# Kernel optimization log

Measured on AMD Instinct MI355X. Metric: run time of the kernel, lower is better.

Reference implementation:

```python
import jax, jax.numpy as jnp
import numpy as np

MU = 0.1            # sinkhorn_mu
SINKHORN_ITERS = 200  # fixed-iteration stand-in for tol=1e-9 loop
M_PTS = 4096
N_PTS = 4096


def l2norm(x, eps=1e-12):
    n = jnp.linalg.norm(x, axis=-1, keepdims=True)
    return x / jnp.maximum(n, eps)


def pairwise_l2(x, y):
    # x: [m,d], y: [n,d] -> [m,n] Euclidean distance
    x2 = jnp.sum(x * x, axis=-1)[:, None]
    y2 = jnp.sum(y * y, axis=-1)[None, :]
    d2 = x2 + y2 - 2.0 * (x @ y.T)
    return jnp.sqrt(jnp.clip(d2, 1e-12, None))


def mlp(x, W1, b1, W2, b2, W3, b3):
    # Linear->Sigmoid x3, torch Linear convention y = x @ W.T + b
    h = jax.nn.sigmoid(x @ W1.T + b1)
    h = jax.nn.sigmoid(h @ W2.T + b2)
    return jax.nn.sigmoid(h @ W3.T + b3)


def sinkhorn(M, r, c):
    # RegularisedTransport: entropic OT, P = diag(u) K diag(v), sum(P)=1
    K = jnp.exp(-M / MU)  # [m,n]
    u0 = jnp.ones_like(r)
    def step(u, _):
        v = c / (K.T @ u)
        u = r / (K @ v)
        return u, None
    u, _ = jax.lax.scan(step, u0, None, length=SINKHORN_ITERS)
    v = c / (K.T @ u)
    return u[:, None] * K * v[None, :]


def setup_inputs() -> dict:
    key = jax.random.key(0)
    ks = jax.random.split(key, 16)
    H, W = 480.0, 640.0
    inp = {
        "sn2d": jax.random.normal(ks[0], (M_PTS, 3), jnp.float32),
        "sn3d": jax.random.normal(ks[1], (N_PTS, 3), jnp.float32),
        "pix2d": jax.random.uniform(ks[2], (M_PTS, 2), jnp.float32) * jnp.array([H, W], jnp.float32),
        "pts3d": jax.random.normal(ks[3], (N_PTS, 3), jnp.float32) * 5.0,
        "intrinsics": jnp.array([[525.0, 0.0, 320.0], [0.0, 525.0, 240.0], [0.0, 0.0, 1.0]], jnp.float32),
    }
    # tiny MLP params (image branch and point branch), torch Linear [out,in]
    dims = [(64, 6), (128, 64), (128, 128)]
    i = 4
    for tag in ("i", "p"):
        for li, (o, c) in enumerate(dims, start=1):
            s = 1.0 / np.sqrt(c)
            inp[f"W{li}{tag}"] = jax.random.uniform(ks[i], (o, c), jnp.float32, -s, s); i += 1
            inp[f"b{li}{tag}"] = jax.random.uniform(ks[i], (o,), jnp.float32, -s, s); i += 1
    return inp


def reference(sn2d, sn3d, pix2d, pts3d, intrinsics,
              W1i, b1i, W2i, b2i, W3i, b3i,
              W1p, b1p, W2p, b2p, W3p, b3p):
    m = pix2d.shape[0]
    n = pts3d.shape[0]
    # normalize surface normals
    sn2d = l2norm(sn2d)
    sn3d = l2norm(sn3d)
    # 2D bearing vectors: [pix, 1] @ inv(K).T, then swap x/y as in source
    tmp = jnp.concatenate([pix2d[:, :2], jnp.ones((m, 1), pix2d.dtype)], axis=1)
    bea = tmp @ jnp.linalg.inv(intrinsics).T
    bea = bea[:, jnp.array([1, 0, 2])]
    nbv2d = l2norm(bea)
    nbv3d = l2norm(pts3d)
    # 6-d features -> tiny MLPs -> L2 normalize
    f2d = l2norm(mlp(jnp.concatenate([sn2d, nbv2d], axis=1), W1i, b1i, W2i, b2i, W3i, b3i))
    f3d = l2norm(mlp(jnp.concatenate([sn3d, nbv3d], axis=1), W1p, b1p, W2p, b2p, W3p, b3p))
    # cost matrix and regularised transport
    Mcost = pairwise_l2(f2d, f3d)  # [m,n]
    r = jnp.full((m,), 1.0 / m, Mcost.dtype)
    c = jnp.full((n,), 1.0 / n, Mcost.dtype)
    P = sinkhorn(Mcost, r, c)
    return P[None]  # [1,m,n]
```

## Files before the change

kernel.cpp:

```cpp
#include <hip/hip_runtime.h>
#include <math.h>

#define NPTS 4096
#define FD   128
#define NITER 200
#define INVN (1.0f / 4096.0f)
#define NBLK 256
#define SMEM_BYTES (NPTS * 4)

typedef unsigned int uint32;
typedef unsigned long long ull;
typedef unsigned int u32x4 __attribute__((ext_vector_type(4)));

__device__ __forceinline__ float sigmoidf_(float x) { return 1.0f / (1.0f + expf(-x)); }

__device__ __forceinline__ unsigned short f2bf(float f) {
    uint32 x = __float_as_uint(f);
    uint32 r = x + 0x7fffu + ((x >> 16) & 1u);
    return (unsigned short)(r >> 16);
}

__device__ __forceinline__ int sgrp(int G) { return G ^ ((G >> 3) & 7); }

__device__ __forceinline__ ull pack2(float a, float b, unsigned gen) {
    return ((ull)(__float_as_uint(a) >> 4) << 36)
         | ((ull)(__float_as_uint(b) >> 4) << 8)
         | (ull)(gen & 0xFFu);
}
__device__ __forceinline__ float unpA(ull x) { return __uint_as_float(((uint32)(x >> 36)) << 4); }
__device__ __forceinline__ float unpB(ull x) { return __uint_as_float(((uint32)(x >> 8))  << 4); }

__device__ __forceinline__ void poll_gen2(const ull* p0, const ull* p1, unsigned expect,
                                          ull& a, ull& b) {
    a = __hip_atomic_load(p0, __ATOMIC_RELAXED, __HIP_MEMORY_SCOPE_AGENT);
    b = __hip_atomic_load(p1, __ATOMIC_RELAXED, __HIP_MEMORY_SCOPE_AGENT);
    int gd = 0;
    while (((unsigned)(a & 0xFFu) != expect) | ((unsigned)(b & 0xFFu) != expect)) {
        __builtin_amdgcn_s_sleep(1);
        if ((unsigned)(a & 0xFFu) != expect)
            a = __hip_atomic_load(p0, __ATOMIC_RELAXED, __HIP_MEMORY_SCOPE_AGENT);
        if ((unsigned)(b & 0xFFu) != expect)
            b = __hip_atomic_load(p1, __ATOMIC_RELAXED, __HIP_MEMORY_SCOPE_AGENT);
        if (++gd > (1 << 24)) break;
    }
}

__device__ __forceinline__ float dpp_sum(float x) {
    asm volatile("v_add_f32 %0, %0, %0 row_shr:1 bound_ctrl:0\n\t"
                 "v_add_f32 %0, %0, %0 row_shr:2 bound_ctrl:0\n\t"
                 "v_add_f32 %0, %0, %0 row_shr:4 bound_ctrl:0\n\t"
                 "v_add_f32 %0, %0, %0 row_shr:8 bound_ctrl:0\n\t"
                 "v_add_f32 %0, %0, %0 row_bcast:15 row_mask:0xa bank_mask:0xf\n\t"
                 "v_add_f32 %0, %0, %0 row_bcast:31 row_mask:0xc bank_mask:0xf"
                 : "+v"(x));
    return x;
}

__device__ __forceinline__ float dot16(u32x4 a, u32x4 b, const float* uu) {
    float acc = 0.0f;
    #pragma unroll
    for (int q = 0; q < 4; ++q)
        acc += __uint_as_float(a[q] << 16)          * uu[2*q]
             + __uint_as_float(a[q] & 0xffff0000u)  * uu[2*q+1];
    #pragma unroll
    for (int q = 0; q < 4; ++q)
        acc += __uint_as_float(b[q] << 16)          * uu[8 + 2*q]
             + __uint_as_float(b[q] & 0xffff0000u)  * uu[8 + 2*q+1];
    return acc;
}

__device__ __forceinline__ float wave_red_sum(float a) {
    #pragma unroll
    for (int m = 32; m >= 1; m >>= 1) a += __shfl_xor(a, m, 64);
    return a;
}

__device__ __forceinline__ float bf16_row_dot(const unsigned short* __restrict__ Krow,
                                              const float* __restrict__ x,
                                              int lane, int first)
{
    const float4* kp = (const float4*)Krow;
    const float4* xp = (const float4*)x;
    float acc = 0.0f;
    #pragma unroll
    for (int s = 0; s < 8; ++s) {
        int i = s*64 + lane;
        float4 kk = kp[i];
        const uint32* kw = (const uint32*)&kk;
        float xx[8];
        if (first) {
            #pragma unroll
            for (int q = 0; q < 8; ++q) xx[q] = 1.0f;
        } else {
            float4 x0 = xp[i*2], x1 = xp[i*2 + 1];
            xx[0]=x0.x; xx[1]=x0.y; xx[2]=x0.z; xx[3]=x0.w;
            xx[4]=x1.x; xx[5]=x1.y; xx[6]=x1.z; xx[7]=x1.w;
        }
        #pragma unroll
        for (int q = 0; q < 4; ++q) {
            acc += __uint_as_float(kw[q] << 16)         * xx[2*q]
                 + __uint_as_float(kw[q] & 0xffff0000u) * xx[2*q+1];
        }
    }
    return acc;
}

__device__ __forceinline__ float f32_row_dot(const float* __restrict__ Krow,
                                             const float* __restrict__ x, int lane)
{
    const float4* kp = (const float4*)Krow;
    const float4* xp = (const float4*)x;
    float acc = 0.0f;
    #pragma unroll
    for (int s = 0; s < 16; ++s) {
        int i = s*64 + lane;
        float4 kk = kp[i], xx = xp[i];
        acc += kk.x*xx.x + kk.y*xx.y + kk.z*xx.z + kk.w*xx.w;
    }
    return acc;
}

__device__ __forceinline__ float f32_col_dot(const float* __restrict__ K,
                                             const float* __restrict__ u,
                                             int col, int lane, int first)
{
    float acc = 0.0f;
    for (int i = lane; i < NPTS; i += 64)
        acc += K[(size_t)i*NPTS + col] * (first ? 1.0f : u[i]);
    return acc;
}

__global__ void feat_kernel(const float* __restrict__ sn2d, const float* __restrict__ sn3d,
                            const float* __restrict__ pix2d, const float* __restrict__ pts3d,
                            const float* __restrict__ intr,
                            const float* __restrict__ W1i, const float* __restrict__ b1i,
                            const float* __restrict__ W2i, const float* __restrict__ b2i,
                            const float* __restrict__ W3i, const float* __restrict__ b3i,
                            const float* __restrict__ W1p, const float* __restrict__ b1p,
                            const float* __restrict__ W2p, const float* __restrict__ b2p,
                            const float* __restrict__ W3p, const float* __restrict__ b3p,
                            float* __restrict__ f2d, float* __restrict__ f3d,
                            float* __restrict__ x2, float* __restrict__ y2)
{
    const int row  = blockIdx.x;
    const int side = blockIdx.y;
    const int tid  = threadIdx.x;

    __shared__ float xin[6];
    __shared__ float h1s[64];
    __shared__ float h2s[128];
    __shared__ float red[2];

    const float* W1 = side ? W1p : W1i;  const float* B1 = side ? b1p : b1i;
    const float* W2 = side ? W2p : W2i;  const float* B2 = side ? b2p : b2i;
    const float* W3 = side ? W3p : W3i;  const float* B3 = side ? b3p : b3i;

    if (tid == 0) {
        if (side == 0) {
            float a0 = sn2d[row*3+0], a1 = sn2d[row*3+1], a2 = sn2d[row*3+2];
            float n = fmaxf(sqrtf(a0*a0 + a1*a1 + a2*a2), 1e-12f);
            xin[0] = a0/n; xin[1] = a1/n; xin[2] = a2/n;
            float m00 = intr[0], m01 = intr[1], m02 = intr[2];
            float m10 = intr[3], m11 = intr[4], m12 = intr[5];
            float m20 = intr[6], m21 = intr[7], m22 = intr[8];
            float det = m00*(m11*m22 - m12*m21) - m01*(m10*m22 - m12*m20) + m02*(m10*m21 - m11*m20);
            float id = 1.0f/det;
            float i00 = (m11*m22 - m12*m21)*id;
            float i01 = (m02*m21 - m01*m22)*id;
            float i02 = (m01*m12 - m02*m11)*id;
            float i10 = (m12*m20 - m10*m22)*id;
            float i11 = (m00*m22 - m02*m20)*id;
            float i12 = (m02*m10 - m00*m12)*id;
            float i20 = (m10*m21 - m11*m20)*id;
            float i21 = (m01*m20 - m00*m21)*id;
            float i22 = (m00*m11 - m01*m10)*id;
            float px = pix2d[row*2+0], py = pix2d[row*2+1];
            float e0 = i00*px + i01*py + i02;
            float e1 = i10*px + i11*py + i12;
            float e2 = i20*px + i21*py + i22;
            float nb = fmaxf(sqrtf(e0*e0 + e1*e1 + e2*e2), 1e-12f);
            xin[3] = e1/nb; xin[4] = e0/nb; xin[5] = e2/nb;
        } else {
            float a0 = sn3d[row*3+0], a1 = sn3d[row*3+1], a2 = sn3d[row*3+2];
            float n = fmaxf(sqrtf(a0*a0 + a1*a1 + a2*a2), 1e-12f);
            xin[0] = a0/n; xin[1] = a1/n; xin[2] = a2/n;
            float p0 = pts3d[row*3+0], p1 = pts3d[row*3+1], p2 = pts3d[row*3+2];
            float pn = fmaxf(sqrtf(p0*p0 + p1*p1 + p2*p2), 1e-12f);
            xin[3] = p0/pn; xin[4] = p1/pn; xin[5] = p2/pn;
        }
    }
    __syncthreads();
    if (tid < 64) {
        float a = B1[tid];
        #pragma unroll
        for (int k = 0; k < 6; ++k) a += xin[k] * W1[tid*6 + k];
        h1s[tid] = sigmoidf_(a);
    }
    __syncthreads();
    {
        float a = B2[tid];
        #pragma unroll 8
        for (int k = 0; k < 64; ++k) a += h1s[k] * W2[tid*64 + k];
        h2s[tid] = sigmoidf_(a);
    }
    __syncthreads();
    float a = B3[tid];
    #pragma unroll 8
    for (int k = 0; k < 128; ++k) a += h2s[k] * W3[tid*128 + k];
    float o = sigmoidf_(a);

    float ss = o*o;
    #pragma unroll
    for (int m = 32; m >= 1; m >>= 1) ss += __shfl_xor(ss, m, 64);
    if ((tid & 63) == 0) red[tid >> 6] = ss;
    __syncthreads();
    float tot = red[0] + red[1];
    float n = fmaxf(sqrtf(tot), 1e-12f);
    float f = o / n;
    (side ? f3d : f2d)[row*FD + tid] = f;

    float ss2 = f*f;
    #pragma unroll
    for (int m = 32; m >= 1; m >>= 1) ss2 += __shfl_xor(ss2, m, 64);
    __syncthreads();
    if ((tid & 63) == 0) red[tid >> 6] = ss2;
    __syncthreads();
    if (tid == 0) (side ? y2 : x2)[row] = red[0] + red[1];
}

__global__ void __launch_bounds__(256) cost_kernel(const float* __restrict__ f2d, const float* __restrict__ f3d,
                                                   const float* __restrict__ x2, const float* __restrict__ y2,
                                                   float* __restrict__ K,
                                                   unsigned short* __restrict__ Kb,
                                                   unsigned short* __restrict__ KbT,
                                                   ull* __restrict__ quv,
                                                   int wantB, int wantT)
{
    __shared__ float As[128][64];
    __shared__ float Bs[128][64];
    const int tid = threadIdx.x;
    const int i0 = blockIdx.y * 64;
    const int j0 = blockIdx.x * 64;

    if (quv && blockIdx.y == 0) {
        int idx = blockIdx.x * 256 + tid;
        if (idx < 4096) quv[idx] = 0ull;
    }

    {
        int r0 = tid >> 5;
        int c  = (tid & 31) * 4;
        for (int rr = r0; rr < 64; rr += 8) {
            float4 av = *(const float4*)(f2d + (size_t)(i0+rr)*FD + c);
            As[c+0][rr] = av.x; As[c+1][rr] = av.y; As[c+2][rr] = av.z; As[c+3][rr] = av.w;
            float4 bv = *(const float4*)(f3d + (size_t)(j0+rr)*FD + c);
            Bs[c+0][rr] = bv.x; Bs[c+1][rr] = bv.y; Bs[c+2][rr] = bv.z; Bs[c+3][rr] = bv.w;
        }
    }
    __syncthreads();

    const int tx = tid & 15;
    const int ty = tid >> 4;
    float acc[4][4] = {};
    for (int k = 0; k < 128; ++k) {
        float4 av = *(const float4*)&As[k][ty*4];
        float4 bv = *(const float4*)&Bs[k][tx*4];
        float aa[4] = {av.x, av.y, av.z, av.w};
        float bb[4] = {bv.x, bv.y, bv.z, bv.w};
        #pragma unroll
        for (int i = 0; i < 4; ++i)
            #pragma unroll
            for (int j = 0; j < 4; ++j)
                acc[i][j] += aa[i] * bb[j];
    }

    float kv[4][4];
    #pragma unroll
    for (int i = 0; i < 4; ++i) {
        int gi = i0 + ty*4 + i;
        float xv = x2[gi];
        #pragma unroll
        for (int j = 0; j < 4; ++j) {
            int gj = j0 + tx*4 + j;
            float d2 = xv + y2[gj] - 2.0f * acc[i][j];
            d2 = fmaxf(d2, 1e-12f);
            kv[i][j] = expf(-sqrtf(d2) * 10.0f);
        }
    }

    #pragma unroll
    for (int i = 0; i < 4; ++i) {
        int gi = i0 + ty*4 + i;
        *(float4*)(K + (size_t)gi*NPTS + j0 + tx*4) = make_float4(kv[i][0], kv[i][1], kv[i][2], kv[i][3]);
        if (wantB) {
            uint32 lo = (uint32)f2bf(kv[i][0]) | ((uint32)f2bf(kv[i][1]) << 16);
            uint32 hi = (uint32)f2bf(kv[i][2]) | ((uint32)f2bf(kv[i][3]) << 16);
            uint2 p; p.x = lo; p.y = hi;
            *(uint2*)(Kb + (size_t)gi*NPTS + j0 + tx*4) = p;
        }
    }
    if (wantT) {
        #pragma unroll
        for (int j = 0; j < 4; ++j) {
            int gj = j0 + tx*4 + j;
            uint32 lo = (uint32)f2bf(kv[0][j]) | ((uint32)f2bf(kv[1][j]) << 16);
            uint32 hi = (uint32)f2bf(kv[2][j]) | ((uint32)f2bf(kv[3][j]) << 16);
            uint2 p; p.x = lo; p.y = hi;
            *(uint2*)(KbT + (size_t)gj*NPTS + i0 + ty*4) = p;
        }
    }
}

__global__ void __launch_bounds__(1024)
__attribute__((amdgpu_waves_per_eu(4, 4)))
sinkhorn_kernel(float* __restrict__ K,
                const unsigned short* __restrict__ Kb,
                const unsigned short* __restrict__ KbT,
                ull* __restrict__ uq,
                ull* __restrict__ vq)
{
    extern __shared__ char smem[];
    float* xs = (float*)smem;
    __shared__ float red[16][4];
    __shared__ float us[16];

    const int tid  = threadIdx.x;
    const int w    = tid >> 6;
    const int lane = tid & 63;
    const int g    = w >> 2;
    const int s    = w & 3;
    const int bid  = blockIdx.x;
    const int base = bid * 16;

    char* xsw = (char*)xs + 16*sgrp(tid);
    int uoff[4];
    #pragma unroll
    for (int k = 0; k < 4; ++k) uoff[k] = 16*sgrp(s*256 + lane*4 + k);

    u32x4 kq[4][2], kt[4][2];
    #pragma unroll
    for (int j = 0; j < 4; ++j) {
        const size_t off = (size_t)(base + 4*g + j) * NPTS + s*1024 + lane*16;
        const u32x4* kp = (const u32x4*)(Kb  + off);
        const u32x4* tp = (const u32x4*)(KbT + off);
        kq[j][0] = kp[0]; kq[j][1] = kp[1];
        kt[j][0] = tp[0]; kt[j][1] = tp[1];
    }

    for (int it = 0; it <= NITER; ++it) {
        #pragma unroll
        for (int j = 0; j < 4; ++j)
            asm volatile("" : "+v"(kq[j][0]), "+v"(kq[j][1]), "+v"(kt[j][0]), "+v"(kt[j][1]));

        if (it == 0) {
            *(float4*)xsw = make_float4(1.f, 1.f, 1.f, 1.f);
        } else {
            ull a, b;
            poll_gen2(&uq[2*tid], &uq[2*tid + 1], (unsigned)it, a, b);
            *(float4*)xsw = make_float4(unpA(a), unpB(a), unpA(b), unpB(b));
        }
        __syncthreads();

        {
            float uu[16];
            #pragma unroll
            for (int k = 0; k < 4; ++k)
                *(float4*)&uu[4*k] = *(const float4*)((const char*)xs + uoff[k]);
            float p[4];
            #pragma unroll
            for (int j = 0; j < 4; ++j) p[j] = dpp_sum(dot16(kt[j][0], kt[j][1], uu));
            if (lane == 63) {
                red[4*g+0][s] = p[0]; red[4*g+1][s] = p[1];
                red[4*g+2][s] = p[2]; red[4*g+3][s] = p[3];
            }
            __syncthreads();
            if (tid < 8) {
                float4 r0 = *(float4*)&red[2*tid][0];
                float4 r1 = *(float4*)&red[2*tid + 1][0];
                float v0 = INVN / (r0.x + r0.y + r0.z + r0.w);
                float v1 = INVN / (r1.x + r1.y + r1.z + r1.w);
                __hip_atomic_store(&vq[bid*8 + tid], pack2(v0, v1, (unsigned)(it + 1)),
                                   __ATOMIC_RELAXED, __HIP_MEMORY_SCOPE_AGENT);
            }
        }
        if (it == NITER) break;

        {
            ull a, b;
            poll_gen2(&vq[2*tid], &vq[2*tid + 1], (unsigned)(it + 1), a, b);
            *(float4*)xsw = make_float4(unpA(a), unpB(a), unpA(b), unpB(b));
        }
        __syncthreads();

        {
            float uu[16];
            #pragma unroll
            for (int k = 0; k < 4; ++k)
                *(float4*)&uu[4*k] = *(const float4*)((const char*)xs + uoff[k]);
            float p[4];
            #pragma unroll
            for (int j = 0; j < 4; ++j) p[j] = dpp_sum(dot16(kq[j][0], kq[j][1], uu));
            if (lane == 63) {
                red[4*g+0][s] = p[0]; red[4*g+1][s] = p[1];
                red[4*g+2][s] = p[2]; red[4*g+3][s] = p[3];
            }
            __syncthreads();
            if (tid < 8) {
                float4 r0 = *(float4*)&red[2*tid][0];
                float4 r1 = *(float4*)&red[2*tid + 1][0];
                float u0 = INVN / (r0.x + r0.y + r0.z + r0.w);
                float u1 = INVN / (r1.x + r1.y + r1.z + r1.w);
                us[2*tid] = u0; us[2*tid + 1] = u1;
                __hip_atomic_store(&uq[bid*8 + tid], pack2(u0, u1, (unsigned)(it + 1)),
                                   __ATOMIC_RELAXED, __HIP_MEMORY_SCOPE_AGENT);
            }
        }
    }

    {
        ull a, b;
        poll_gen2(&vq[2*tid], &vq[2*tid + 1], (unsigned)(NITER + 1), a, b);
        *(float4*)xsw = make_float4(unpA(a), unpB(a), unpA(b), unpB(b));
        __syncthreads();

        const float ur = us[w];
        float4* kp = (float4*)(K + (size_t)(base + w) * NPTS);
        #pragma unroll
        for (int t = 0; t < 16; ++t) {
            int G = t*64 + lane;
            float4 kk = kp[G];
            float4 vv = *(const float4*)((const char*)xs + 16*sgrp(G));
            kk.x *= ur * vv.x; kk.y *= ur * vv.y; kk.z *= ur * vv.z; kk.w *= ur * vv.w;
            kp[G] = kk;
        }
    }
}

__global__ void __launch_bounds__(1024) stepA_kernel(const float* __restrict__ K,
                                                     const unsigned short* __restrict__ KbT,
                                                     const float* __restrict__ u, float* __restrict__ v,
                                                     int first, int modeA)
{
    const int w = threadIdx.x >> 6, lane = threadIdx.x & 63;
    const int r = blockIdx.x * 16 + w;
    float acc = modeA ? bf16_row_dot(KbT + (size_t)r * NPTS, u, lane, first)
                      : f32_col_dot(K, u, r, lane, first);
    acc = wave_red_sum(acc);
    if (lane == 0) v[r] = INVN / acc;
}

__global__ void __launch_bounds__(1024) stepB_kernel(const float* __restrict__ K,
                                                     const unsigned short* __restrict__ Kb,
                                                     const float* __restrict__ v, float* __restrict__ u,
                                                     int modeB)
{
    const int w = threadIdx.x >> 6, lane = threadIdx.x & 63;
    const int r = blockIdx.x * 16 + w;
    float acc = modeB ? bf16_row_dot(Kb + (size_t)r * NPTS, v, lane, 0)
                      : f32_row_dot(K + (size_t)r * NPTS, v, lane);
    acc = wave_red_sum(acc);
    if (lane == 0) u[r] = INVN / acc;
}

__global__ void __launch_bounds__(1024) final_kernel(float* __restrict__ K,
                                                     const float* __restrict__ u,
                                                     const float* __restrict__ v)
{
    const int w = threadIdx.x >> 6, lane = threadIdx.x & 63;
    const int r = blockIdx.x * 16 + w;
    const float ur = u[r];
    float4* kp = (float4*)(K + (size_t)r * NPTS);
    const float4* vp = (const float4*)v;
    #pragma unroll
    for (int s = 0; s < 16; ++s) {
        int e4 = s * 64 + lane;
        float4 kk = kp[e4], vv = vp[e4];
        kk.x *= ur * vv.x; kk.y *= ur * vv.y; kk.z *= ur * vv.z; kk.w *= ur * vv.w;
        kp[e4] = kk;
    }
}

extern "C" void kernel_launch(void* const* d_in, const int* in_sizes, int n_in,
                              void* d_out, int out_size, void* d_ws, size_t ws_size,
                              hipStream_t stream)
{
    (void)in_sizes; (void)n_in; (void)out_size;
    const float* sn2d  = (const float*)d_in[0];
    const float* sn3d  = (const float*)d_in[1];
    const float* pix2d = (const float*)d_in[2];
    const float* pts3d = (const float*)d_in[3];
    const float* intr  = (const float*)d_in[4];
    const float* W1i = (const float*)d_in[5];  const float* b1i = (const float*)d_in[6];
    const float* W2i = (const float*)d_in[7];  const float* b2i = (const float*)d_in[8];
    const float* W3i = (const float*)d_in[9];  const float* b3i = (const float*)d_in[10];
    const float* W1p = (const float*)d_in[11]; const float* b1p = (const float*)d_in[12];
    const float* W2p = (const float*)d_in[13]; const float* b2p = (const float*)d_in[14];
    const float* W3p = (const float*)d_in[15]; const float* b3p = (const float*)d_in[16];

    float* ws  = (float*)d_ws;
    float* f2d = ws;
    float* f3d = f2d + NPTS*FD;
    float* x2  = f3d + NPTS*FD;
    float* y2  = x2 + NPTS;
    float* uf  = y2 + NPTS;
    float* vf  = uf + NPTS;
    ull*   uq  = (ull*)(vf + NPTS);
    ull*   vq  = uq + NPTS/2;
    unsigned short* KbT = (unsigned short*)(vq + NPTS/2);
    unsigned short* Kb  = KbT + (size_t)NPTS*NPTS;
    float* K   = (float*)d_out;

    const size_t base_bytes = (size_t)(2*NPTS*FD + 4*NPTS) * 4 + (size_t)2*NPTS*4 + (size_t)NPTS*8;
    const size_t bf16_bytes = (size_t)NPTS * NPTS * 2;
    const size_t need_full  = base_bytes + 2*bf16_bytes;
    int coop_ok = (ws_size >= need_full) ? 1 : 0;
    int modeA = (ws_size >= base_bytes + bf16_bytes)   ? 1 : 0;
    int modeB = (ws_size >= base_bytes + 2*bf16_bytes) ? 1 : 0;

    feat_kernel<<<dim3(NPTS, 2), 128, 0, stream>>>(sn2d, sn3d, pix2d, pts3d, intr,
        W1i, b1i, W2i, b2i, W3i, b3i, W1p, b1p, W2p, b2p, W3p, b3p,
        f2d, f3d, x2, y2);

    cost_kernel<<<dim3(64, 64), 256, 0, stream>>>(f2d, f3d, x2, y2, K, Kb, KbT,
                                                  coop_ok ? uq : (ull*)0,
                                                  modeB, modeA);

    hipError_t err = hipErrorUnknown;
    if (coop_ok) {
        void* args[] = { (void*)&K, (void*)&Kb, (void*)&KbT, (void*)&uq, (void*)&vq };
        err = hipLaunchCooperativeKernel((const void*)sinkhorn_kernel,
                                         dim3(NBLK), dim3(1024), args, SMEM_BYTES, stream);
    }
    if (err != hipSuccess) {
        stepA_kernel<<<256, 1024, 0, stream>>>(K, KbT, uf, vf, 1, modeA);
        for (int i = 0; i < NITER; ++i) {
            stepB_kernel<<<256, 1024, 0, stream>>>(K, Kb, vf, uf, modeB);
            stepA_kernel<<<256, 1024, 0, stream>>>(K, KbT, uf, vf, 0, modeA);
        }
        final_kernel<<<256, 1024, 0, stream>>>(K, uf, vf);
    }
}
```

Baseline: 1.515 ms.

## Switch register-resident Sinkhorn kernel to fp16 with scaled vectors and fdot2

Stores the bf16 kernel copies as fp16 instead, and also keeps the u/v scaling vectors in shared memory as packed fp16. The scale factor is folded in through exponent offsets (XSCALE/FINC, plus 2^10 in the unpack), and values are clamped below the fp16 maximum. The inner dot products become v_dot2 fp16 instructions instead of bf16 unpack-and-multiply, which halves LDS traffic for the vectors and cuts ALU work per iteration. The fallback path loses its bf16 modes and uses only fp32. There is a risk of fp16 overflow or underflow in the scaled vectors hurting accuracy.

```diff
diff --git a/kernel.cpp b/kernel.cpp
--- a/kernel.cpp
+++ b/kernel.cpp
@@ -6,21 +6,24 @@
 #define NITER 200
 #define INVN (1.0f / 4096.0f)
 #define NBLK 256
+#define XSCALE 1024.0f
+#define FINC 0.25f
 #define SMEM_BYTES (NPTS * 4)
 
 typedef unsigned int uint32;
 typedef unsigned long long ull;
 typedef unsigned int u32x4 __attribute__((ext_vector_type(4)));
+typedef __fp16 h2v __attribute__((ext_vector_type(2)));
 
 __device__ __forceinline__ float sigmoidf_(float x) { return 1.0f / (1.0f + expf(-x)); }
 
-__device__ __forceinline__ unsigned short f2bf(float f) {
-    uint32 x = __float_as_uint(f);
-    uint32 r = x + 0x7fffu + ((x >> 16) & 1u);
-    return (unsigned short)(r >> 16);
+__device__ __forceinline__ uint32 pkh(float a, float b) {
+    h2v h = __builtin_amdgcn_cvt_pkrtz(a, b);
+    return __builtin_bit_cast(uint32, h);
 }
 
 __device__ __forceinline__ int sgrp(int G) { return G ^ ((G >> 3) & 7); }
+__device__ __forceinline__ int swz2(int G) { return G ^ ((G >> 2) & 3); }
 
 __device__ __forceinline__ ull pack2(float a, float b, unsigned gen) {
     return ((ull)(__float_as_uint(a) >> 4) << 36)
@@ -29,6 +32,8 @@
 }
 __device__ __forceinline__ float unpA(ull x) { return __uint_as_float(((uint32)(x >> 36)) << 4); }
 __device__ __forceinline__ float unpB(ull x) { return __uint_as_float(((uint32)(x >> 8))  << 4); }
+__device__ __forceinline__ float unpAs(ull x) { return __uint_as_float((((uint32)(x >> 36)) << 4) + (10u << 23)); }
+__device__ __forceinline__ float unpBs(ull x) { return __uint_as_float((((uint32)(x >> 8))  << 4) + (10u << 23)); }
 
 __device__ __forceinline__ void poll_gen2(const ull* p0, const ull* p1, unsigned expect,
                                           ull& a, ull& b) {
@@ -56,16 +61,16 @@
     return x;
 }
 
-__device__ __forceinline__ float dot16(u32x4 a, u32x4 b, const float* uu) {
+__device__ __forceinline__ float dot16h(u32x4 a, u32x4 b, u32x4 x0, u32x4 x1) {
     float acc = 0.0f;
     #pragma unroll
     for (int q = 0; q < 4; ++q)
-        acc += __uint_as_float(a[q] << 16)          * uu[2*q]
-             + __uint_as_float(a[q] & 0xffff0000u)  * uu[2*q+1];
+        acc = __builtin_amdgcn_fdot2(__builtin_bit_cast(h2v, a[q]),
+                                     __builtin_bit_cast(h2v, x0[q]), acc, false);
     #pragma unroll
     for (int q = 0; q < 4; ++q)
-        acc += __uint_as_float(b[q] << 16)          * uu[8 + 2*q]
-             + __uint_as_float(b[q] & 0xffff0000u)  * uu[8 + 2*q+1];
+        acc = __builtin_amdgcn_fdot2(__builtin_bit_cast(h2v, b[q]),
+                                     __builtin_bit_cast(h2v, x1[q]), acc, false);
     return acc;
 }
 
@@ -73,36 +78,6 @@
     #pragma unroll
     for (int m = 32; m >= 1; m >>= 1) a += __shfl_xor(a, m, 64);
     return a;
-}
-
-__device__ __forceinline__ float bf16_row_dot(const unsigned short* __restrict__ Krow,
-                                              const float* __restrict__ x,
-                                              int lane, int first)
-{
-    const float4* kp = (const float4*)Krow;
-    const float4* xp = (const float4*)x;
-    float acc = 0.0f;
-    #pragma unroll
-    for (int s = 0; s < 8; ++s) {
-        int i = s*64 + lane;
-        float4 kk = kp[i];
-        const uint32* kw = (const uint32*)&kk;
-        float xx[8];
-        if (first) {
-            #pragma unroll
-            for (int q = 0; q < 8; ++q) xx[q] = 1.0f;
-        } else {
-            float4 x0 = xp[i*2], x1 = xp[i*2 + 1];
-            xx[0]=x0.x; xx[1]=x0.y; xx[2]=x0.z; xx[3]=x0.w;
-            xx[4]=x1.x; xx[5]=x1.y; xx[6]=x1.z; xx[7]=x1.w;
-        }
-        #pragma unroll
-        for (int q = 0; q < 4; ++q) {
-            acc += __uint_as_float(kw[q] << 16)         * xx[2*q]
-                 + __uint_as_float(kw[q] & 0xffff0000u) * xx[2*q+1];
-        }
-    }
-    return acc;
 }
 
 __device__ __forceinline__ float f32_row_dot(const float* __restrict__ Krow,
@@ -293,9 +268,7 @@
         int gi = i0 + ty*4 + i;
         *(float4*)(K + (size_t)gi*NPTS + j0 + tx*4) = make_float4(kv[i][0], kv[i][1], kv[i][2], kv[i][3]);
         if (wantB) {
-            uint32 lo = (uint32)f2bf(kv[i][0]) | ((uint32)f2bf(kv[i][1]) << 16);
-            uint32 hi = (uint32)f2bf(kv[i][2]) | ((uint32)f2bf(kv[i][3]) << 16);
-            uint2 p; p.x = lo; p.y = hi;
+            uint2 p; p.x = pkh(kv[i][0], kv[i][1]); p.y = pkh(kv[i][2], kv[i][3]);
             *(uint2*)(Kb + (size_t)gi*NPTS + j0 + tx*4) = p;
         }
     }
@@ -303,9 +276,7 @@
         #pragma unroll
         for (int j = 0; j < 4; ++j) {
             int gj = j0 + tx*4 + j;
-            uint32 lo = (uint32)f2bf(kv[0][j]) | ((uint32)f2bf(kv[1][j]) << 16);
-            uint32 hi = (uint32)f2bf(kv[2][j]) | ((uint32)f2bf(kv[3][j]) << 16);
-            uint2 p; p.x = lo; p.y = hi;
+            uint2 p; p.x = pkh(kv[0][j], kv[1][j]); p.y = pkh(kv[2][j], kv[3][j]);
             *(uint2*)(KbT + (size_t)gj*NPTS + i0 + ty*4) = p;
         }
     }
@@ -332,10 +303,9 @@
     const int bid  = blockIdx.x;
     const int base = bid * 16;
 
-    char* xsw = (char*)xs + 16*sgrp(tid);
-    int uoff[4];
-    #pragma unroll
-    for (int k = 0; k < 4; ++k) uoff[k] = 16*sgrp(s*256 + lane*4 + k);
+    char* xsw2 = (char*)xs + 16*swz2(tid >> 1) + 8*(tid & 1);
+    const int xoff0 = 16*swz2(s*128 + 2*lane);
+    const int xoff1 = 16*swz2(s*128 + 2*lane + 1);
 
     u32x4 kq[4][2], kt[4][2];
     #pragma unroll
@@ -353,22 +323,24 @@
             asm volatile("" : "+v"(kq[j][0]), "+v"(kq[j][1]), "+v"(kt[j][0]), "+v"(kt[j][1]));
 
         if (it == 0) {
-            *(float4*)xsw = make_float4(1.f, 1.f, 1.f, 1.f);
+            uint32 o1 = pkh(XSCALE, XSCALE);
+            *(ull*)xsw2 = ((ull)o1 << 32) | o1;
         } else {
             ull a, b;
             poll_gen2(&uq[2*tid], &uq[2*tid + 1], (unsigned)it, a, b);
-            *(float4*)xsw = make_float4(unpA(a), unpB(a), unpA(b), unpB(b));
+            float f0 = fminf(unpAs(a), 60000.f), f1 = fminf(unpBs(a), 60000.f);
+            float f2 = fminf(unpAs(b), 60000.f), f3 = fminf(unpBs(b), 60000.f);
+            uint32 w0 = pkh(f0, f1), w1 = pkh(f2, f3);
+            *(ull*)xsw2 = ((ull)w1 << 32) | w0;
         }
         __syncthreads();
 
         {
-            float uu[16];
-            #pragma unroll
-            for (int k = 0; k < 4; ++k)
-                *(float4*)&uu[4*k] = *(const float4*)((const char*)xs + uoff[k]);
+            u32x4 x0 = *(const u32x4*)((const char*)xs + xoff0);
+            u32x4 x1 = *(const u32x4*)((const char*)xs + xoff1);
             float p[4];
             #pragma unroll
-            for (int j = 0; j < 4; ++j) p[j] = dpp_sum(dot16(kt[j][0], kt[j][1], uu));
+            for (int j = 0; j < 4; ++j) p[j] = dpp_sum(dot16h(kt[j][0], kt[j][1], x0, x1));
             if (lane == 63) {
                 red[4*g+0][s] = p[0]; red[4*g+1][s] = p[1];
                 red[4*g+2][s] = p[2]; red[4*g+3][s] = p[3];
@@ -377,8 +349,8 @@
             if (tid < 8) {
                 float4 r0 = *(float4*)&red[2*tid][0];
                 float4 r1 = *(float4*)&red[2*tid + 1][0];
-                float v0 = INVN / (r0.x + r0.y + r0.z + r0.w);
-                float v1 = INVN / (r1.x + r1.y + r1.z + r1.w);
+                float v0 = FINC / (r0.x + r0.y + r0.z + r0.w);
+                float v1 = FINC / (r1.x + r1.y + r1.z + r1.w);
                 __hip_atomic_store(&vq[bid*8 + tid], pack2(v0, v1, (unsigned)(it + 1)),
                                    __ATOMIC_RELAXED, __HIP_MEMORY_SCOPE_AGENT);
             }
@@ -388,18 +360,19 @@
         {
             ull a, b;
             poll_gen2(&vq[2*tid], &vq[2*tid + 1], (unsigned)(it + 1), a, b);
-            *(float4*)xsw = make_float4(unpA(a), unpB(a), unpA(b), unpB(b));
+            float f0 = fminf(unpAs(a), 60000.f), f1 = fminf(unpBs(a), 60000.f);
+            float f2 = fminf(unpAs(b), 60000.f), f3 = fminf(unpBs(b), 60000.f);
+            uint32 w0 = pkh(f0, f1), w1 = pkh(f2, f3);
+            *(ull*)xsw2 = ((ull)w1 << 32) | w0;
         }
         __syncthreads();
 
         {
-            float uu[16];
-            #pragma unroll
-            for (int k = 0; k < 4; ++k)
-                *(float4*)&uu[4*k] = *(const float4*)((const char*)xs + uoff[k]);
+            u32x4 x0 = *(const u32x4*)((const char*)xs + xoff0);
+            u32x4 x1 = *(const u32x4*)((const char*)xs + xoff1);
             float p[4];
             #pragma unroll
-            for (int j = 0; j < 4; ++j) p[j] = dpp_sum(dot16(kq[j][0], kq[j][1], uu));
+            for (int j = 0; j < 4; ++j) p[j] = dpp_sum(dot16h(kq[j][0], kq[j][1], x0, x1));
             if (lane == 63) {
                 red[4*g+0][s] = p[0]; red[4*g+1][s] = p[1];
                 red[4*g+2][s] = p[2]; red[4*g+3][s] = p[3];
@@ -408,8 +381,8 @@
             if (tid < 8) {
                 float4 r0 = *(float4*)&red[2*tid][0];
                 float4 r1 = *(float4*)&red[2*tid + 1][0];
-                float u0 = INVN / (r0.x + r0.y + r0.z + r0.w);
-                float u1 = INVN / (r1.x + r1.y + r1.z + r1.w);
+                float u0 = FINC / (r0.x + r0.y + r0.z + r0.w);
+                float u1 = FINC / (r1.x + r1.y + r1.z + r1.w);
                 us[2*tid] = u0; us[2*tid + 1] = u1;
                 __hip_atomic_store(&uq[bid*8 + tid], pack2(u0, u1, (unsigned)(it + 1)),
                                    __ATOMIC_RELAXED, __HIP_MEMORY_SCOPE_AGENT);
@@ -420,7 +393,7 @@
     {
         ull a, b;
         poll_gen2(&vq[2*tid], &vq[2*tid + 1], (unsigned)(NITER + 1), a, b);
-        *(float4*)xsw = make_float4(unpA(a), unpB(a), unpA(b), unpB(b));
+        *(float4*)((char*)xs + 16*sgrp(tid)) = make_float4(unpA(a), unpB(a), unpA(b), unpB(b));
         __syncthreads();
 
         const float ur = us[w];
@@ -437,27 +410,22 @@
 }
 
 __global__ void __launch_bounds__(1024) stepA_kernel(const float* __restrict__ K,
-                                                     const unsigned short* __restrict__ KbT,
                                                      const float* __restrict__ u, float* __restrict__ v,
-                                                     int first, int modeA)
+                                                     int first)
 {
     const int w = threadIdx.x >> 6, lane = threadIdx.x & 63;
     const int r = blockIdx.x * 16 + w;
-    float acc = modeA ? bf16_row_dot(KbT + (size_t)r * NPTS, u, lane, first)
-                      : f32_col_dot(K, u, r, lane, first);
+    float acc = f32_col_dot(K, u, r, lane, first);
     acc = wave_red_sum(acc);
     if (lane == 0) v[r] = INVN / acc;
 }
 
 __global__ void __launch_bounds__(1024) stepB_kernel(const float* __restrict__ K,
-                                                     const unsigned short* __restrict__ Kb,
-                                                     const float* __restrict__ v, float* __restrict__ u,
-                                                     int modeB)
+                                                     const float* __restrict__ v, float* __restrict__ u)
 {
     const int w = threadIdx.x >> 6, lane = threadIdx.x & 63;
     const int r = blockIdx.x * 16 + w;
-    float acc = modeB ? bf16_row_dot(Kb + (size_t)r * NPTS, v, lane, 0)
-                      : f32_row_dot(K + (size_t)r * NPTS, v, lane);
+    float acc = f32_row_dot(K + (size_t)r * NPTS, v, lane);
     acc = wave_red_sum(acc);
     if (lane == 0) u[r] = INVN / acc;
 }
@@ -511,11 +479,11 @@
     float* K   = (float*)d_out;
 
     const size_t base_bytes = (size_t)(2*NPTS*FD + 4*NPTS) * 4 + (size_t)2*NPTS*4 + (size_t)NPTS*8;
-    const size_t bf16_bytes = (size_t)NPTS * NPTS * 2;
-    const size_t need_full  = base_bytes + 2*bf16_bytes;
+    const size_t f16_bytes  = (size_t)NPTS * NPTS * 2;
+    const size_t need_full  = base_bytes + 2*f16_bytes;
     int coop_ok = (ws_size >= need_full) ? 1 : 0;
-    int modeA = (ws_size >= base_bytes + bf16_bytes)   ? 1 : 0;
-    int modeB = (ws_size >= base_bytes + 2*bf16_bytes) ? 1 : 0;
+    int wantT = (ws_size >= base_bytes + f16_bytes)   ? 1 : 0;
+    int wantB = (ws_size >= base_bytes + 2*f16_bytes) ? 1 : 0;
 
     feat_kernel<<<dim3(NPTS, 2), 128, 0, stream>>>(sn2d, sn3d, pix2d, pts3d, intr,
         W1i, b1i, W2i, b2i, W3i, b3i, W1p, b1p, W2p, b2p, W3p, b3p,
@@ -523,7 +491,7 @@
 
     cost_kernel<<<dim3(64, 64), 256, 0, stream>>>(f2d, f3d, x2, y2, K, Kb, KbT,
                                                   coop_ok ? uq : (ull*)0,
-                                                  modeB, modeA);
+                                                  wantB, wantT);
 
     hipError_t err = hipErrorUnknown;
     if (coop_ok) {
@@ -532,10 +500,10 @@
                                          dim3(NBLK), dim3(1024), args, SMEM_BYTES, stream);
     }
     if (err != hipSuccess) {
-        stepA_kernel<<<256, 1024, 0, stream>>>(K, KbT, uf, vf, 1, modeA);
+        stepA_kernel<<<256, 1024, 0, stream>>>(K, uf, vf, 1);
         for (int i = 0; i < NITER; ++i) {
-            stepB_kernel<<<256, 1024, 0, stream>>>(K, Kb, vf, uf, modeB);
-            stepA_kernel<<<256, 1024, 0, stream>>>(K, KbT, uf, vf, 0, modeA);
+            stepB_kernel<<<256, 1024, 0, stream>>>(K, vf, uf);
+            stepA_kernel<<<256, 1024, 0, stream>>>(K, uf, vf, 0);
         }
         final_kernel<<<256, 1024, 0, stream>>>(K, uf, vf);
     }
```

Result: faster. 1.443 ms (-4.8%).
